# Kernel tuning notes

Measured on AMD Instinct MI355X. Metric: run time of the kernel, lower is better.

Reference implementation:

```python
import jax, jax.numpy as jnp
import numpy as np

NUM_USERS = 100000
NUM_ITEMS = 100000
EMBED_DIM = 64
BATCH = 4096
MAX_NEIGH = 50


def setup_inputs() -> dict:
    key = jax.random.key(0)
    ks = jax.random.split(key, 12)
    d = EMBED_DIM
    nodes = jax.random.randint(ks[0], (BATCH,), 0, NUM_USERS)
    neighbors = jax.random.randint(ks[1], (BATCH, MAX_NEIGH), 0, NUM_ITEMS)
    lengths = 1 + jax.random.randint(ks[2], (BATCH,), 0, MAX_NEIGH)  # ragged sizes in [1, MAX_NEIGH]
    u_table = jax.random.normal(ks[3], (NUM_USERS, d), dtype=jnp.float32) * 0.1
    i_table = jax.random.normal(ks[4], (NUM_ITEMS, d), dtype=jnp.float32) * 0.1
    # GraphRec-style attention MLP: Linear(2d,d) -> relu -> Linear(d,d) -> relu -> Linear(d,1) -> softmax
    W1 = jax.random.normal(ks[5], (2 * d, d), dtype=jnp.float32) * (1.0 / np.sqrt(2 * d))
    b1 = jnp.zeros((d,), dtype=jnp.float32)
    W2 = jax.random.normal(ks[6], (d, d), dtype=jnp.float32) * (1.0 / np.sqrt(d))
    b2 = jnp.zeros((d,), dtype=jnp.float32)
    W3 = jax.random.normal(ks[7], (d, 1), dtype=jnp.float32) * (1.0 / np.sqrt(d))
    b3 = jnp.zeros((1,), dtype=jnp.float32)
    return {"u_table": u_table, "i_table": i_table, "W1": W1, "b1": b1,
            "W2": W2, "b2": b2, "W3": W3, "b3": b3,
            "nodes": nodes, "neighbors": neighbors, "lengths": lengths}


def reference(u_table, i_table, W1, b1, W2, b2, W3, b3, nodes, neighbors, lengths):
    # is_user=True: gather item features for neighbors, user feature for the node itself.
    neighs = i_table[neighbors]            # [B, L, d]
    node = u_table[nodes]                  # [B, d]
    B, L, d = neighs.shape
    x = jnp.concatenate([neighs, jnp.broadcast_to(node[:, None, :], (B, L, d))], axis=-1)  # [B, L, 2d]
    h = jax.nn.relu(x @ W1 + b1)           # [B, L, d]
    h = jax.nn.relu(h @ W2 + b2)           # [B, L, d]
    logits = (h @ W3 + b3)[..., 0]         # [B, L]
    mask = jnp.arange(L)[None, :] < lengths[:, None]  # ragged neighbor mask
    logits = jnp.where(mask, logits, -jnp.inf)
    att = jax.nn.softmax(logits, axis=1)   # softmax over each node's neighbors (dim=0 per-node in torch)
    # embedding = (neighs^T att)^T  ==  sum_l att[b,l] * neighs[b,l,:]
    return jnp.einsum("bl,bld->bd", att, neighs)  # [B, d]
```

## Files before the change

kernel.cpp:

```cpp
#include <hip/hip_runtime.h>
#include <math.h>

#define NB    4096
#define LMAX  50
#define NWAVE 2048

typedef short bf16x8 __attribute__((ext_vector_type(8)));
typedef float f32x4  __attribute__((ext_vector_type(4)));

__device__ __forceinline__ short f2bf(float f) {
    union { float f; unsigned u; } v; v.f = f;
    unsigned r = v.u + 0x7FFFu + ((v.u >> 16) & 1u);
    return (short)(r >> 16);
}
__device__ __forceinline__ float bf2f(short s) {
    union { unsigned u; float f; } v; v.u = ((unsigned)(unsigned short)s) << 16;
    return v.f;
}
__device__ __forceinline__ bf16x8 cvt8(const float* __restrict__ p) {
    const float4* q = (const float4*)p;
    float4 x = q[0], y = q[1];
    bf16x8 r;
    r[0] = f2bf(x.x); r[1] = f2bf(x.y); r[2] = f2bf(x.z); r[3] = f2bf(x.w);
    r[4] = f2bf(y.x); r[5] = f2bf(y.y); r[6] = f2bf(y.z); r[7] = f2bf(y.w);
    return r;
}

__global__ __launch_bounds__(256) void graphrec_wave_kernel(
    const float* __restrict__ u_table,
    const float* __restrict__ i_table,
    const float* __restrict__ W1, const float* __restrict__ b1,
    const float* __restrict__ W2, const float* __restrict__ b2,
    const float* __restrict__ W3, const float* __restrict__ b3,
    const int* __restrict__ nodes,
    const int* __restrict__ neighbors,
    const int* __restrict__ lengths,
    float* __restrict__ out)
{
    __shared__ __attribute__((aligned(16))) short WLDS[24][64][8];
    __shared__ __attribute__((aligned(16))) unsigned short Hs[4][16 * 72];
    __shared__ float Ls[4][16];

    const int tid  = threadIdx.x;
    const int w    = tid >> 6;
    const int lane = tid & 63;
    const int l15  = lane & 15;
    const int g    = lane >> 4;

    for (int f = w; f < 24; f += 4) {
        const float* Wsrc = (f < 16) ? W1 : W2;
        const int    fi   = (f < 16) ? f : f - 16;
        const int    ks   = fi >> 2, nt = fi & 3;
        bf16x8 fr;
        #pragma unroll
        for (int i = 0; i < 8; ++i)
            fr[i] = f2bf(Wsrc[(ks * 32 + g * 8 + i) * 64 + nt * 16 + l15]);
        *(bf16x8*)&WLDS[f][lane][0] = fr;
    }
    __syncthreads();

    bf16x8 w1f[4][4], w2f[2][4];
    #pragma unroll
    for (int ks = 0; ks < 4; ++ks)
        #pragma unroll
        for (int nt = 0; nt < 4; ++nt)
            w1f[ks][nt] = *(const bf16x8*)&WLDS[ks * 4 + nt][lane][0];
    #pragma unroll
    for (int ks = 0; ks < 2; ++ks)
        #pragma unroll
        for (int nt = 0; nt < 4; ++nt)
            w2f[ks][nt] = *(const bf16x8*)&WLDS[16 + ks * 4 + nt][lane][0];

    float b1v[4], b2v[4], w3v[4];
    #pragma unroll
    for (int nt = 0; nt < 4; ++nt) {
        b1v[nt] = b1[nt * 16 + l15];
        b2v[nt] = b2[nt * 16 + l15];
        w3v[nt] = W3[nt * 16 + l15];
    }

    const int wid = blockIdx.x * 4 + w;

    for (int kk = 0; kk < 2; ++kk) {
        const int b    = wid + kk * NWAVE;
        const int len  = lengths[b];
        const int node = nodes[b];

        bf16x8 axu0 = cvt8(u_table + node * 64 +      g * 8);
        bf16x8 axu1 = cvt8(u_table + node * 64 + 32 + g * 8);
        f32x4 hn[4];
        #pragma unroll
        for (int nt = 0; nt < 4; ++nt)
            hn[nt] = (f32x4){b1v[nt], b1v[nt], b1v[nt], b1v[nt]};
        #pragma unroll
        for (int nt = 0; nt < 4; ++nt)
            hn[nt] = __builtin_amdgcn_mfma_f32_16x16x32_bf16(axu0, w1f[2][nt], hn[nt], 0, 0, 0);
        #pragma unroll
        for (int nt = 0; nt < 4; ++nt)
            hn[nt] = __builtin_amdgcn_mfma_f32_16x16x32_bf16(axu1, w1f[3][nt], hn[nt], 0, 0, 0);

        float m = -INFINITY, ssum = 0.f;
        float accW[16];
        #pragma unroll
        for (int i = 0; i < 16; ++i) accW[i] = 0.f;

        const int ntile = (len + 15) >> 4;
        for (int t = 0; t < ntile; ++t) {
            const int  r  = t * 16 + l15;
            const bool vr = (r < len);
            bf16x8 a0 = {0,0,0,0,0,0,0,0}, a1 = {0,0,0,0,0,0,0,0};
            if (vr) {
                const int nbr = neighbors[b * LMAX + r];
                a0 = cvt8(i_table + nbr * 64 +      g * 8);
                a1 = cvt8(i_table + nbr * 64 + 32 + g * 8);
            }

            f32x4 acc[4];
            #pragma unroll
            for (int nt = 0; nt < 4; ++nt) acc[nt] = hn[nt];
            #pragma unroll
            for (int nt = 0; nt < 4; ++nt)
                acc[nt] = __builtin_amdgcn_mfma_f32_16x16x32_bf16(a0, w1f[0][nt], acc[nt], 0, 0, 0);
            #pragma unroll
            for (int nt = 0; nt < 4; ++nt)
                acc[nt] = __builtin_amdgcn_mfma_f32_16x16x32_bf16(a1, w1f[1][nt], acc[nt], 0, 0, 0);

            #pragma unroll
            for (int nt = 0; nt < 4; ++nt)
                #pragma unroll
                for (int reg = 0; reg < 4; ++reg)
                    Hs[w][(g * 4 + reg) * 72 + nt * 16 + l15] =
                        (unsigned short)f2bf(fmaxf(acc[nt][reg], 0.f));
            bf16x8 h0 = *(const bf16x8*)&Hs[w][l15 * 72 +      g * 8];
            bf16x8 h1 = *(const bf16x8*)&Hs[w][l15 * 72 + 32 + g * 8];

            f32x4 c2[4];
            #pragma unroll
            for (int nt = 0; nt < 4; ++nt)
                c2[nt] = (f32x4){b2v[nt], b2v[nt], b2v[nt], b2v[nt]};
            #pragma unroll
            for (int nt = 0; nt < 4; ++nt)
                c2[nt] = __builtin_amdgcn_mfma_f32_16x16x32_bf16(h0, w2f[0][nt], c2[nt], 0, 0, 0);
            #pragma unroll
            for (int nt = 0; nt < 4; ++nt)
                c2[nt] = __builtin_amdgcn_mfma_f32_16x16x32_bf16(h1, w2f[1][nt], c2[nt], 0, 0, 0);

            float sv[4];
            #pragma unroll
            for (int reg = 0; reg < 4; ++reg) {
                float s = 0.f;
                #pragma unroll
                for (int nt = 0; nt < 4; ++nt)
                    s = fmaf(fmaxf(c2[nt][reg], 0.f), w3v[nt], s);
                #pragma unroll
                for (int off = 1; off < 16; off <<= 1) s += __shfl_xor(s, off);
                if (t * 16 + g * 4 + reg >= len) s = -INFINITY;
                sv[reg] = s;
            }

            float tm = fmaxf(fmaxf(sv[0], sv[1]), fmaxf(sv[2], sv[3]));
            tm = fmaxf(tm, __shfl_xor(tm, 16));
            tm = fmaxf(tm, __shfl_xor(tm, 32));
            if (tm > m) {
                const float nm = fmaxf(m, tm);
                const float sc = __expf(m - nm);
                ssum *= sc;
                #pragma unroll
                for (int i = 0; i < 16; ++i) accW[i] *= sc;
                m = nm;
            }
            float e0 = __expf(sv[0] - m), e1 = __expf(sv[1] - m);
            float e2 = __expf(sv[2] - m), e3 = __expf(sv[3] - m);
            float es = (e0 + e1) + (e2 + e3);
            es += __shfl_xor(es, 16);
            es += __shfl_xor(es, 32);
            ssum += es;

            if (l15 == 0) {
                float4 t4 = make_float4(e0, e1, e2, e3);
                *(float4*)&Ls[w][g * 4] = t4;
            }
            const float er = Ls[w][l15];

            #pragma unroll
            for (int i = 0; i < 8; ++i) accW[i]     = fmaf(er, bf2f(a0[i]), accW[i]);
            #pragma unroll
            for (int i = 0; i < 8; ++i) accW[8 + i] = fmaf(er, bf2f(a1[i]), accW[8 + i]);
        }

        #pragma unroll
        for (int i = 0; i < 16; ++i) {
            #pragma unroll
            for (int off = 1; off < 16; off <<= 1)
                accW[i] += __shfl_xor(accW[i], off);
        }
        const float inv = 1.f / ssum;
        if (l15 == 0) {
            float4 o0 = make_float4(accW[0] * inv,  accW[1] * inv,  accW[2] * inv,  accW[3] * inv);
            float4 o1 = make_float4(accW[4] * inv,  accW[5] * inv,  accW[6] * inv,  accW[7] * inv);
            float4 o2 = make_float4(accW[8] * inv,  accW[9] * inv,  accW[10] * inv, accW[11] * inv);
            float4 o3 = make_float4(accW[12] * inv, accW[13] * inv, accW[14] * inv, accW[15] * inv);
            *(float4*)(out + b * 64 +      g * 8)     = o0;
            *(float4*)(out + b * 64 +      g * 8 + 4) = o1;
            *(float4*)(out + b * 64 + 32 + g * 8)     = o2;
            *(float4*)(out + b * 64 + 32 + g * 8 + 4) = o3;
        }
    }
}

extern "C" void kernel_launch(void* const* d_in, const int* in_sizes, int n_in,
                              void* d_out, int out_size, void* d_ws, size_t ws_size,
                              hipStream_t stream) {
    const float* u_table   = (const float*)d_in[0];
    const float* i_table   = (const float*)d_in[1];
    const float* W1        = (const float*)d_in[2];
    const float* b1        = (const float*)d_in[3];
    const float* W2        = (const float*)d_in[4];
    const float* b2        = (const float*)d_in[5];
    const float* W3        = (const float*)d_in[6];
    const float* b3        = (const float*)d_in[7];
    const int*   nodes     = (const int*)d_in[8];
    const int*   neighbors = (const int*)d_in[9];
    const int*   lengths   = (const int*)d_in[10];
    float* out = (float*)d_out;

    graphrec_wave_kernel<<<dim3(NWAVE / 4), dim3(256), 0, stream>>>(
        u_table, i_table, W1, b1, W2, b2, W3, b3, nodes, neighbors, lengths, out);
}
```

Before: 25.82 us.

## Prefetch neighbor indices and double-buffer gathers; use hardware bf16 pack conversion

Loads all neighbor indices and both user rows up front, then software-pipelines the item-table gathers two tiles ahead inside a fully unrolled tile loop. Float-to-bf16 conversions use the v_cvt_pk_bf16_f32 instruction instead of manual bit-rounding. The aim is to hide gather latency behind the MFMA work and to cut ALU cost. The trade-off is higher register pressure, and it hardcodes at most 4 tiles, which is valid only because LMAX is 50.

Result: faster. 22.83 us (-11.6%).

```diff
diff --git a/kernel.cpp b/kernel.cpp
--- a/kernel.cpp
+++ b/kernel.cpp
@@ -1,119 +1,70 @@
 #include <hip/hip_runtime.h>
 #include <math.h>
 
-#define NB    4096
 #define LMAX  50
 #define NWAVE 2048
 
 typedef short bf16x8 __attribute__((ext_vector_type(8)));
 typedef float f32x4  __attribute__((ext_vector_type(4)));
-
-__device__ __forceinline__ short f2bf(float f) {
-    union { float f; unsigned u; } v; v.f = f;
-    unsigned r = v.u + 0x7FFFu + ((v.u >> 16) & 1u);
-    return (short)(r >> 16);
-}
-__device__ __forceinline__ float bf2f(short s) {
-    union { unsigned u; float f; } v; v.u = ((unsigned)(unsigned short)s) << 16;
-    return v.f;
-}
-__device__ __forceinline__ bf16x8 cvt8(const float* __restrict__ p) {
-    const float4* q = (const float4*)p;
-    float4 x = q[0], y = q[1];
-    bf16x8 r;
-    r[0] = f2bf(x.x); r[1] = f2bf(x.y); r[2] = f2bf(x.z); r[3] = f2bf(x.w);
-    r[4] = f2bf(y.x); r[5] = f2bf(y.y); r[6] = f2bf(y.z); r[7] = f2bf(y.w);
+union bfu { bf16x8 v; unsigned u[4]; };
+
+__device__ __forceinline__ unsigned cvt_pk(float lo, float hi) {
+    unsigned r;
+    asm("v_cvt_pk_bf16_f32 %0, %1, %2" : "=v"(r) : "v"(lo), "v"(hi));
     return r;
 }
-
-__global__ __launch_bounds__(256) void graphrec_wave_kernel(
-    const float* __restrict__ u_table,
-    const float* __restrict__ i_table,
-    const float* __restrict__ W1, const float* __restrict__ b1,
-    const float* __restrict__ W2, const float* __restrict__ b2,
-    const float* __restrict__ W3, const float* __restrict__ b3,
-    const int* __restrict__ nodes,
-    const int* __restrict__ neighbors,
-    const int* __restrict__ lengths,
-    float* __restrict__ out)
+__device__ __forceinline__ bf16x8 cvt8f(float4 a, float4 b) {
+    bfu r;
+    r.u[0] = cvt_pk(a.x, a.y); r.u[1] = cvt_pk(a.z, a.w);
+    r.u[2] = cvt_pk(b.x, b.y); r.u[3] = cvt_pk(b.z, b.w);
+    return r.v;
+}
+
+__device__ __forceinline__ void process_elem(
+    const float* __restrict__ i_table, float* __restrict__ out,
+    int b, int len, const int (&idx)[6],
+    bf16x8 axu0, bf16x8 axu1,
+    const bf16x8 (&w1f)[4][4], const bf16x8 (&w2f)[2][4],
+    const float (&b1v)[4], const float (&b2v)[4], const float (&w3v)[4],
+    unsigned short* __restrict__ hw, float* __restrict__ Lsw,
+    int l15, int g)
 {
-    __shared__ __attribute__((aligned(16))) short WLDS[24][64][8];
-    __shared__ __attribute__((aligned(16))) unsigned short Hs[4][16 * 72];
-    __shared__ float Ls[4][16];
-
-    const int tid  = threadIdx.x;
-    const int w    = tid >> 6;
-    const int lane = tid & 63;
-    const int l15  = lane & 15;
-    const int g    = lane >> 4;
-
-    for (int f = w; f < 24; f += 4) {
-        const float* Wsrc = (f < 16) ? W1 : W2;
-        const int    fi   = (f < 16) ? f : f - 16;
-        const int    ks   = fi >> 2, nt = fi & 3;
-        bf16x8 fr;
-        #pragma unroll
-        for (int i = 0; i < 8; ++i)
-            fr[i] = f2bf(Wsrc[(ks * 32 + g * 8 + i) * 64 + nt * 16 + l15]);
-        *(bf16x8*)&WLDS[f][lane][0] = fr;
-    }
-    __syncthreads();
-
-    bf16x8 w1f[4][4], w2f[2][4];
-    #pragma unroll
-    for (int ks = 0; ks < 4; ++ks)
-        #pragma unroll
-        for (int nt = 0; nt < 4; ++nt)
-            w1f[ks][nt] = *(const bf16x8*)&WLDS[ks * 4 + nt][lane][0];
-    #pragma unroll
-    for (int ks = 0; ks < 2; ++ks)
-        #pragma unroll
-        for (int nt = 0; nt < 4; ++nt)
-            w2f[ks][nt] = *(const bf16x8*)&WLDS[16 + ks * 4 + nt][lane][0];
-
-    float b1v[4], b2v[4], w3v[4];
-    #pragma unroll
-    for (int nt = 0; nt < 4; ++nt) {
-        b1v[nt] = b1[nt * 16 + l15];
-        b2v[nt] = b2[nt * 16 + l15];
-        w3v[nt] = W3[nt * 16 + l15];
-    }
-
-    const int wid = blockIdx.x * 4 + w;
-
-    for (int kk = 0; kk < 2; ++kk) {
-        const int b    = wid + kk * NWAVE;
-        const int len  = lengths[b];
-        const int node = nodes[b];
-
-        bf16x8 axu0 = cvt8(u_table + node * 64 +      g * 8);
-        bf16x8 axu1 = cvt8(u_table + node * 64 + 32 + g * 8);
-        f32x4 hn[4];
-        #pragma unroll
-        for (int nt = 0; nt < 4; ++nt)
-            hn[nt] = (f32x4){b1v[nt], b1v[nt], b1v[nt], b1v[nt]};
-        #pragma unroll
-        for (int nt = 0; nt < 4; ++nt)
-            hn[nt] = __builtin_amdgcn_mfma_f32_16x16x32_bf16(axu0, w1f[2][nt], hn[nt], 0, 0, 0);
-        #pragma unroll
-        for (int nt = 0; nt < 4; ++nt)
-            hn[nt] = __builtin_amdgcn_mfma_f32_16x16x32_bf16(axu1, w1f[3][nt], hn[nt], 0, 0, 0);
-
-        float m = -INFINITY, ssum = 0.f;
-        float accW[16];
-        #pragma unroll
-        for (int i = 0; i < 16; ++i) accW[i] = 0.f;
-
-        const int ntile = (len + 15) >> 4;
-        for (int t = 0; t < ntile; ++t) {
-            const int  r  = t * 16 + l15;
-            const bool vr = (r < len);
-            bf16x8 a0 = {0,0,0,0,0,0,0,0}, a1 = {0,0,0,0,0,0,0,0};
-            if (vr) {
-                const int nbr = neighbors[b * LMAX + r];
-                a0 = cvt8(i_table + nbr * 64 +      g * 8);
-                a1 = cvt8(i_table + nbr * 64 + 32 + g * 8);
-            }
+    const int g8    = g * 8;
+    const int ntile = (len + 15) >> 4;
+
+    float4 LA[2][4];
+    #define ISSUE_T(t) if ((t) < ntile) { \
+        const float* xp = i_table + (size_t)idx[t] * 64 + g8; \
+        LA[(t) & 1][0] = *(const float4*)(xp); \
+        LA[(t) & 1][1] = *(const float4*)(xp + 4); \
+        LA[(t) & 1][2] = *(const float4*)(xp + 32); \
+        LA[(t) & 1][3] = *(const float4*)(xp + 36); \
+    }
+    ISSUE_T(0)
+    ISSUE_T(1)
+
+    f32x4 hn[4];
+    #pragma unroll
+    for (int nt = 0; nt < 4; ++nt)
+        hn[nt] = (f32x4){b1v[nt], b1v[nt], b1v[nt], b1v[nt]};
+    #pragma unroll
+    for (int nt = 0; nt < 4; ++nt)
+        hn[nt] = __builtin_amdgcn_mfma_f32_16x16x32_bf16(axu0, w1f[2][nt], hn[nt], 0, 0, 0);
+    #pragma unroll
+    for (int nt = 0; nt < 4; ++nt)
+        hn[nt] = __builtin_amdgcn_mfma_f32_16x16x32_bf16(axu1, w1f[3][nt], hn[nt], 0, 0, 0);
+
+    float m = -INFINITY, ssum = 0.f;
+    float accW[16];
+    #pragma unroll
+    for (int i = 0; i < 16; ++i) accW[i] = 0.f;
+
+    #pragma unroll
+    for (int t = 0; t < 4; ++t) {
+        if (t < ntile) {
+            bf16x8 a0 = cvt8f(LA[t & 1][0], LA[t & 1][1]);
+            bf16x8 a1 = cvt8f(LA[t & 1][2], LA[t & 1][3]);
+            if (t + 2 < 4) ISSUE_T(t + 2)
 
             f32x4 acc[4];
             #pragma unroll
@@ -126,13 +77,16 @@
                 acc[nt] = __builtin_amdgcn_mfma_f32_16x16x32_bf16(a1, w1f[1][nt], acc[nt], 0, 0, 0);
 
             #pragma unroll
-            for (int nt = 0; nt < 4; ++nt)
-                #pragma unroll
-                for (int reg = 0; reg < 4; ++reg)
-                    Hs[w][(g * 4 + reg) * 72 + nt * 16 + l15] =
-                        (unsigned short)f2bf(fmaxf(acc[nt][reg], 0.f));
-            bf16x8 h0 = *(const bf16x8*)&Hs[w][l15 * 72 +      g * 8];
-            bf16x8 h1 = *(const bf16x8*)&Hs[w][l15 * 72 + 32 + g * 8];
+            for (int nt = 0; nt < 4; ++nt) {
+                unsigned p0 = cvt_pk(fmaxf(acc[nt][0], 0.f), fmaxf(acc[nt][1], 0.f));
+                unsigned p1 = cvt_pk(fmaxf(acc[nt][2], 0.f), fmaxf(acc[nt][3], 0.f));
+                hw[(g * 4 + 0) * 72 + nt * 16 + l15] = (unsigned short)p0;
+                hw[(g * 4 + 1) * 72 + nt * 16 + l15] = (unsigned short)(p0 >> 16);
+                hw[(g * 4 + 2) * 72 + nt * 16 + l15] = (unsigned short)p1;
+                hw[(g * 4 + 3) * 72 + nt * 16 + l15] = (unsigned short)(p1 >> 16);
+            }
+            bf16x8 h0 = *(const bf16x8*)&hw[l15 * 72 + g8];
+            bf16x8 h1 = *(const bf16x8*)&hw[l15 * 72 + 32 + g8];
 
             f32x4 c2[4];
             #pragma unroll
@@ -152,8 +106,8 @@
                 #pragma unroll
                 for (int nt = 0; nt < 4; ++nt)
                     s = fmaf(fmaxf(c2[nt][reg], 0.f), w3v[nt], s);
-                #pragma unroll
-                for (int off = 1; off < 16; off <<= 1) s += __shfl_xor(s, off);
+                s += __shfl_xor(s, 1); s += __shfl_xor(s, 2);
+                s += __shfl_xor(s, 4); s += __shfl_xor(s, 8);
                 if (t * 16 + g * 4 + reg >= len) s = -INFINITY;
                 sv[reg] = s;
             }
@@ -162,7 +116,7 @@
             tm = fmaxf(tm, __shfl_xor(tm, 16));
             tm = fmaxf(tm, __shfl_xor(tm, 32));
             if (tm > m) {
-                const float nm = fmaxf(m, tm);
+                const float nm = tm;
                 const float sc = __expf(m - nm);
                 ssum *= sc;
                 #pragma unroll
@@ -176,36 +130,128 @@
             es += __shfl_xor(es, 32);
             ssum += es;
 
-            if (l15 == 0) {
-                float4 t4 = make_float4(e0, e1, e2, e3);
-                *(float4*)&Ls[w][g * 4] = t4;
-            }
-            const float er = Ls[w][l15];
-
-            #pragma unroll
-            for (int i = 0; i < 8; ++i) accW[i]     = fmaf(er, bf2f(a0[i]), accW[i]);
-            #pragma unroll
-            for (int i = 0; i < 8; ++i) accW[8 + i] = fmaf(er, bf2f(a1[i]), accW[8 + i]);
+            if (l15 == 0) *(float4*)&Lsw[g * 4] = make_float4(e0, e1, e2, e3);
+            const float er = Lsw[l15];
+
+            #pragma unroll
+            for (int i = 0; i < 8; ++i) {
+                union { unsigned u; float f; } lo, hi2;
+                lo.u  = ((unsigned)(unsigned short)a0[i]) << 16;
+                hi2.u = ((unsigned)(unsigned short)a1[i]) << 16;
+                accW[i]     = fmaf(er, lo.f,  accW[i]);
+                accW[8 + i] = fmaf(er, hi2.f, accW[8 + i]);
+            }
         }
-
+    }
+    #undef ISSUE_T
+
+    #pragma unroll
+    for (int i = 0; i < 16; ++i) {
+        accW[i] += __shfl_xor(accW[i], 1);
+        accW[i] += __shfl_xor(accW[i], 2);
+        accW[i] += __shfl_xor(accW[i], 4);
+        accW[i] += __shfl_xor(accW[i], 8);
+    }
+    const float inv = 1.f / ssum;
+    if (l15 == 0) {
+        float4 o0 = make_float4(accW[0] * inv,  accW[1] * inv,  accW[2] * inv,  accW[3] * inv);
+        float4 o1 = make_float4(accW[4] * inv,  accW[5] * inv,  accW[6] * inv,  accW[7] * inv);
+        float4 o2 = make_float4(accW[8] * inv,  accW[9] * inv,  accW[10] * inv, accW[11] * inv);
+        float4 o3 = make_float4(accW[12] * inv, accW[13] * inv, accW[14] * inv, accW[15] * inv);
+        *(float4*)(out + b * 64 +      g8)     = o0;
+        *(float4*)(out + b * 64 +      g8 + 4) = o1;
+        *(float4*)(out + b * 64 + 32 + g8)     = o2;
+        *(float4*)(out + b * 64 + 32 + g8 + 4) = o3;
+    }
+}
+
+__global__ __launch_bounds__(256, 2) void graphrec_k(
+    const float* __restrict__ u_table, const float* __restrict__ i_table,
+    const float* __restrict__ W1, const float* __restrict__ b1,
+    const float* __restrict__ W2, const float* __restrict__ b2,
+    const float* __restrict__ W3, const float* __restrict__ b3,
+    const int* __restrict__ nodes, const int* __restrict__ neighbors,
+    const int* __restrict__ lengths, float* __restrict__ out)
+{
+    __shared__ __attribute__((aligned(16))) short WL[24][64][8];
+    __shared__ __attribute__((aligned(16))) unsigned short Hs[4][16 * 72];
+    __shared__ float Ls[4][16];
+
+    const int tid  = threadIdx.x;
+    const int w    = tid >> 6, lane = tid & 63;
+    const int l15  = lane & 15, g = lane >> 4, g8 = g * 8;
+
+    for (int f = w; f < 24; f += 4) {
+        const float* Ws = (f < 16) ? W1 : W2;
+        const int    fi = (f < 16) ? f : f - 16;
+        const int    ks = fi >> 2, nt = fi & 3;
+        const float* p  = Ws + (ks * 32 + g8) * 64 + nt * 16 + l15;
+        bfu r;
+        r.u[0] = cvt_pk(p[0 * 64], p[1 * 64]);
+        r.u[1] = cvt_pk(p[2 * 64], p[3 * 64]);
+        r.u[2] = cvt_pk(p[4 * 64], p[5 * 64]);
+        r.u[3] = cvt_pk(p[6 * 64], p[7 * 64]);
+        *(bf16x8*)&WL[f][lane][0] = r.v;
+    }
+    __syncthreads();
+
+    bf16x8 w1f[4][4], w2f[2][4];
+    #pragma unroll
+    for (int ks = 0; ks < 4; ++ks)
         #pragma unroll
-        for (int i = 0; i < 16; ++i) {
-            #pragma unroll
-            for (int off = 1; off < 16; off <<= 1)
-                accW[i] += __shfl_xor(accW[i], off);
-        }
-        const float inv = 1.f / ssum;
-        if (l15 == 0) {
-            float4 o0 = make_float4(accW[0] * inv,  accW[1] * inv,  accW[2] * inv,  accW[3] * inv);
-            float4 o1 = make_float4(accW[4] * inv,  accW[5] * inv,  accW[6] * inv,  accW[7] * inv);
-            float4 o2 = make_float4(accW[8] * inv,  accW[9] * inv,  accW[10] * inv, accW[11] * inv);
-            float4 o3 = make_float4(accW[12] * inv, accW[13] * inv, accW[14] * inv, accW[15] * inv);
-            *(float4*)(out + b * 64 +      g * 8)     = o0;
-            *(float4*)(out + b * 64 +      g * 8 + 4) = o1;
-            *(float4*)(out + b * 64 + 32 + g * 8)     = o2;
-            *(float4*)(out + b * 64 + 32 + g * 8 + 4) = o3;
-        }
-    }
+        for (int nt = 0; nt < 4; ++nt)
+            w1f[ks][nt] = *(const bf16x8*)&WL[ks * 4 + nt][lane][0];
+    #pragma unroll
+    for (int ks = 0; ks < 2; ++ks)
+        #pragma unroll
+        for (int nt = 0; nt < 4; ++nt)
+            w2f[ks][nt] = *(const bf16x8*)&WL[16 + ks * 4 + nt][lane][0];
+
+    float b1v[4], b2v[4], w3v[4];
+    #pragma unroll
+    for (int nt = 0; nt < 4; ++nt) {
+        b1v[nt] = b1[nt * 16 + l15];
+        b2v[nt] = b2[nt * 16 + l15];
+        w3v[nt] = W3[nt * 16 + l15];
+    }
+
+    const int wid = blockIdx.x * 4 + w;
+    const int b0  = wid, b1e = wid + NWAVE;
+
+    const int len0 = lengths[b0], len1 = lengths[b1e];
+    const int nd0  = nodes[b0],   nd1  = nodes[b1e];
+
+    int idx0[6] = {0, 0, 0, 0, 0, 0}, idx1[6] = {0, 0, 0, 0, 0, 0};
+    const int nt0 = (len0 + 15) >> 4, nt1 = (len1 + 15) >> 4;
+    #pragma unroll
+    for (int t = 0; t < 4; ++t) {
+        int r = t * 16 + l15; if (r >= len0) r = len0 - 1;
+        if (t < nt0) idx0[t] = neighbors[b0 * LMAX + r];
+    }
+    #pragma unroll
+    for (int t = 0; t < 4; ++t) {
+        int r = t * 16 + l15; if (r >= len1) r = len1 - 1;
+        if (t < nt1) idx1[t] = neighbors[b1e * LMAX + r];
+    }
+
+    const float* up0 = u_table + (size_t)nd0 * 64 + g8;
+    const float* up1 = u_table + (size_t)nd1 * 64 + g8;
+    float4 U00 = *(const float4*)(up0);
+    float4 U01 = *(const float4*)(up0 + 4);
+    float4 U02 = *(const float4*)(up0 + 32);
+    float4 U03 = *(const float4*)(up0 + 36);
+    float4 U10 = *(const float4*)(up1);
+    float4 U11 = *(const float4*)(up1 + 4);
+    float4 U12 = *(const float4*)(up1 + 32);
+    float4 U13 = *(const float4*)(up1 + 36);
+
+    process_elem(i_table, out, b0, len0, idx0,
+                 cvt8f(U00, U01), cvt8f(U02, U03),
+                 w1f, w2f, b1v, b2v, w3v, &Hs[w][0], &Ls[w][0], l15, g);
+
+    process_elem(i_table, out, b1e, len1, idx1,
+                 cvt8f(U10, U11), cvt8f(U12, U13),
+                 w1f, w2f, b1v, b2v, w3v, &Hs[w][0], &Ls[w][0], l15, g);
 }
 
 extern "C" void kernel_launch(void* const* d_in, const int* in_sizes, int n_in,
@@ -224,6 +270,6 @@
     const int*   lengths   = (const int*)d_in[10];
     float* out = (float*)d_out;
 
-    graphrec_wave_kernel<<<dim3(NWAVE / 4), dim3(256), 0, stream>>>(
+    graphrec_k<<<dim3(NWAVE / 4), dim3(256), 0, stream>>>(
         u_table, i_table, W1, b1, W2, b2, W3, b3, nodes, neighbors, lengths, out);
 }
```
